# Optimization experiments

Hardware: AMD Instinct MI355X
Metric: run time of the kernel (lower is better)

## Reference

```python
import jax, jax.numpy as jnp
import numpy as np

STATE_MASS = 4.0
EPS = 1e-5
LOW_RANK_SCALE = 0.1  # _LOW_RANK_SCALE_INIT


def _ln(x, g, b):
    mu = jnp.mean(x, axis=-1, keepdims=True)
    var = jnp.var(x, axis=-1, keepdims=True)
    return (x - mu) * jax.lax.rsqrt(var + EPS) * g + b


def _signed_abs_softmax(s, axis=-1):
    s = jnp.nan_to_num(s)
    return jnp.sign(s) * jax.nn.softmax(jnp.abs(s), axis=axis)


def _signed_softmax_state(st):
    st = jnp.nan_to_num(st)
    return jnp.sign(st) * jax.nn.softmax(jnp.abs(st), axis=-1) * STATE_MASS


def _low_rank_scores(dst, src, Ut_w, Ut_b, Us_w, Us_b, w):
    # bilinear low-rank pairwise: score[b,i,j] = sum_r (dst_i Ut)_r * w_r * (src_j Us)_r
    pt = dst @ Ut_w + Ut_b                      # [B,Nd,R]
    ps = src @ Us_w + Us_b                      # [B,Ns,R]
    return jnp.einsum('bir,r,bjr->bij', pt, w * LOW_RANK_SCALE, ps)


def _gather_rows(x, idx):
    # x: [B,N,...], idx: [B,M,K] -> [B,M,K,...] (per-batch gather, no NxM broadcast)
    return jax.vmap(lambda xi, ii: xi[ii])(x, idx)


def setup_inputs() -> dict:
    key = jax.random.key(0)
    ks = jax.random.split(key, 8)
    B, S, D, M, R = 16, 2048, 512, 256, 64
    std = 0.02
    return {
        'token_val': jax.random.normal(ks[0], (B, S, D), jnp.float32),
        'token_state': jax.random.normal(ks[1], (B, S), jnp.float32),
        'init_state': jax.random.normal(ks[2], (M,), jnp.float32) * std,
        'init_val': jax.random.normal(ks[3], (M, D), jnp.float32) * std,
        'rUs_w': jax.random.normal(ks[4], (D, R), jnp.float32) * std,
        'rUs_b': jnp.zeros((R,), jnp.float32),
        'rUt_w': jax.random.normal(ks[5], (D, R), jnp.float32) * std,
        'rUt_b': jnp.zeros((R,), jnp.float32),
        'r_w': jnp.ones((R,), jnp.float32),
        'pUs_w': jax.random.normal(ks[6], (D, R), jnp.float32) * std,
        'pUs_b': jnp.zeros((R,), jnp.float32),
        'pUt_w': jax.random.normal(ks[7], (D, R), jnp.float32) * std,
        'pUt_b': jnp.zeros((R,), jnp.float32),
        'p_w': jnp.ones((R,), jnp.float32),
        'ln_g': jnp.ones((D,), jnp.float32),
        'ln_b': jnp.zeros((D,), jnp.float32),
        'topk': 16,
    }


def reference(token_val, token_state, init_state, init_val,
              rUs_w, rUs_b, rUt_w, rUt_b, r_w,
              pUs_w, pUs_b, pUt_w, pUt_b, p_w,
              ln_g, ln_b, topk):
    B = token_val.shape[0]
    M, D = init_val.shape

    # _MemoryLevel.initialize
    mem_state = _signed_softmax_state(jnp.broadcast_to(init_state, (B, M)))
    mem_val = _ln(jnp.broadcast_to(init_val, (B, M, D)), ln_g, ln_b)

    # ---- SparseTransition (write): route tokens -> slots, top-k sources/slot ----
    scores = _low_rank_scores(mem_val, token_val, rUt_w, rUt_b, rUs_w, rUs_b, r_w)  # [B,M,S]
    _, idx = jax.lax.top_k(jnp.abs(scores), topk)              # [B,M,K]
    sel = jnp.take_along_axis(scores, idx, axis=-1)            # [B,M,K]
    edges = _signed_abs_softmax(sel, axis=-1)                  # signed-abs-softmax over edges
    v_sel = _gather_rows(token_val, idx)                       # [B,M,K,D]
    s_sel = _gather_rows(token_state, idx)                     # [B,M,K]
    mem_val = mem_val + jnp.einsum('bmk,bmkd->bmd', edges, v_sel)   # merge_mode='add'
    mem_state = mem_state + jnp.einsum('bmk,bmk->bm', edges, s_sel)
    mem_state = _signed_softmax_state(mem_state)
    mem_val = _ln(mem_val, ln_g, ln_b)

    # ---- SparsePropagation within slots: state-weighted top-k edges, residual ----
    pscores = _low_rank_scores(mem_val, mem_val, pUt_w, pUt_b, pUs_w, pUs_b, p_w)   # [B,M,M]
    pscores = pscores * mem_state[:, None, :]                  # state_weight_edges
    _, pidx = jax.lax.top_k(jnp.abs(pscores), topk)            # [B,M,K]
    psel = jnp.take_along_axis(pscores, pidx, axis=-1)
    pe = _signed_abs_softmax(psel, axis=-1)
    pv = _gather_rows(mem_val, pidx)                           # [B,M,K,D]
    pst = _gather_rows(mem_state, pidx)                        # [B,M,K]
    mem_val = mem_val + jnp.einsum('bmk,bmkd->bmd', pe, pv)    # residual=True
    mem_state = mem_state + jnp.einsum('bmk,bmk->bm', pe, pst)
    mem_state = _signed_softmax_state(mem_state)
    mem_val = _ln(mem_val, ln_g, ln_b)
    return mem_val
```

## Files before the change

### kernel.cpp

```cpp
#include <hip/hip_runtime.h>
#include <hip/hip_bf16.h>
#include <math.h>

#define BB 16
#define SS 2048
#define DD 512
#define MM 256
#define RR 64
#define KK 16
#define GPAD 68

__device__ __forceinline__ float wave_sum(float v) {
#pragma unroll
  for (int off = 32; off > 0; off >>= 1) v += __shfl_xor(v, off);
  return v;
}

__device__ __forceinline__ float sgnf(float v) {
  return (v > 0.f) ? 1.f : ((v < 0.f) ? -1.f : 0.f);
}

__global__ __launch_bounds__(256) void k_init(
    const float* __restrict__ init_val, const float* __restrict__ ln_g,
    const float* __restrict__ ln_b, const float* __restrict__ rUt_w,
    const float* __restrict__ rUt_b, const float* __restrict__ r_w,
    float* __restrict__ mv0, float* __restrict__ pt0) {
  int m = blockIdx.x, t = threadIdx.x;
  __shared__ float row[DD];
  __shared__ float red[8];
  float x0 = init_val[m * DD + t];
  float x1 = init_val[m * DD + t + 256];
  float s = wave_sum(x0 + x1);
  float sq = wave_sum(x0 * x0 + x1 * x1);
  if ((t & 63) == 0) { red[t >> 6] = s; red[4 + (t >> 6)] = sq; }
  __syncthreads();
  float mean = (red[0] + red[1] + red[2] + red[3]) * (1.0f / DD);
  float var = (red[4] + red[5] + red[6] + red[7]) * (1.0f / DD) - mean * mean;
  float rs = rsqrtf(var + 1e-5f);
  float n0 = (x0 - mean) * rs * ln_g[t] + ln_b[t];
  float n1 = (x1 - mean) * rs * ln_g[t + 256] + ln_b[t + 256];
  mv0[m * DD + t] = n0;
  mv0[m * DD + t + 256] = n1;
  row[t] = n0;
  row[t + 256] = n1;
  __syncthreads();
  if (t < RR) {
    float acc = rUt_b[t];
    for (int d = 0; d < DD; ++d) acc += row[d] * rUt_w[d * RR + t];
    pt0[m * RR + t] = acc * r_w[t] * 0.1f;
  }
}

__global__ __launch_bounds__(256) void k_state_softmax(
    const float* __restrict__ in, float* __restrict__ out) {
  int b = blockIdx.x, t = threadIdx.x;
  __shared__ float red[4];
  float v = in[b * MM + t];
  float a = fabsf(v);
  float mx = a;
#pragma unroll
  for (int off = 32; off > 0; off >>= 1) mx = fmaxf(mx, __shfl_xor(mx, off));
  if ((t & 63) == 0) red[t >> 6] = mx;
  __syncthreads();
  mx = fmaxf(fmaxf(red[0], red[1]), fmaxf(red[2], red[3]));
  __syncthreads();
  float e = expf(a - mx);
  float ssum = wave_sum(e);
  if ((t & 63) == 0) red[t >> 6] = ssum;
  __syncthreads();
  ssum = red[0] + red[1] + red[2] + red[3];
  out[b * MM + t] = sgnf(v) * e / ssum * 4.0f;
}

__global__ __launch_bounds__(256) void k_ps(
    const float* __restrict__ A, const float* __restrict__ W,
    const float* __restrict__ bias, float* __restrict__ C0,
    float* __restrict__ C1) {
  __shared__ float Ast[32][256];
  __shared__ float Ws[32][RR];
  int t = threadIdx.x;
  int cg = t & 7;
  int rg = t >> 3;
  int half = blockIdx.x >> 7;
  int row0 = (blockIdx.x & 127) * 256;
  int k0 = half * 256;
  float* C = half ? C1 : C0;
  float4 ra[8];
  float4 rw[2];
#pragma unroll
  for (int i = 0; i < 8; ++i)
    ra[i] = *reinterpret_cast<const float4*>(
        &A[(size_t)(row0 + t) * DD + k0 + i * 4]);
#pragma unroll
  for (int i = 0; i < 2; ++i) {
    int slot = i * 256 + t;
    int k = slot >> 4, c4 = slot & 15;
    rw[i] = *reinterpret_cast<const float4*>(&W[(size_t)(k0 + k) * RR + c4 * 4]);
  }
  float acc[8][8] = {};
  for (int c = 0; c < 8; ++c) {
    __syncthreads();
#pragma unroll
    for (int i = 0; i < 8; ++i) {
      Ast[i * 4 + 0][t] = ra[i].x;
      Ast[i * 4 + 1][t] = ra[i].y;
      Ast[i * 4 + 2][t] = ra[i].z;
      Ast[i * 4 + 3][t] = ra[i].w;
    }
#pragma unroll
    for (int i = 0; i < 2; ++i) {
      int slot = i * 256 + t;
      int k = slot >> 4, c4 = slot & 15;
      *reinterpret_cast<float4*>(&Ws[k][c4 * 4]) = rw[i];
    }
    __syncthreads();
    if (c < 7) {
      int kc = k0 + (c + 1) * 32;
#pragma unroll
      for (int i = 0; i < 8; ++i)
        ra[i] = *reinterpret_cast<const float4*>(
            &A[(size_t)(row0 + t) * DD + kc + i * 4]);
#pragma unroll
      for (int i = 0; i < 2; ++i) {
        int slot = i * 256 + t;
        int k = slot >> 4, c4 = slot & 15;
        rw[i] = *reinterpret_cast<const float4*>(
            &W[(size_t)(kc + k) * RR + c4 * 4]);
      }
    }
#pragma unroll
    for (int k = 0; k < 32; ++k) {
      float4 a0 = *reinterpret_cast<const float4*>(&Ast[k][rg * 8]);
      float4 a1 = *reinterpret_cast<const float4*>(&Ast[k][rg * 8 + 4]);
      float4 w0 = *reinterpret_cast<const float4*>(&Ws[k][cg * 8]);
      float4 w1 = *reinterpret_cast<const float4*>(&Ws[k][cg * 8 + 4]);
      float av[8] = {a0.x, a0.y, a0.z, a0.w, a1.x, a1.y, a1.z, a1.w};
      float wv[8] = {w0.x, w0.y, w0.z, w0.w, w1.x, w1.y, w1.z, w1.w};
#pragma unroll
      for (int r = 0; r < 8; ++r)
#pragma unroll
        for (int cc = 0; cc < 8; ++cc) acc[r][cc] += av[r] * wv[cc];
    }
  }
  float bvx[8];
#pragma unroll
  for (int cc = 0; cc < 8; ++cc) bvx[cc] = (half == 0) ? bias[cg * 8 + cc] : 0.f;
#pragma unroll
  for (int r = 0; r < 8; ++r) {
    int rr = row0 + rg * 8 + r;
    float4 o0, o1;
    o0.x = acc[r][0] + bvx[0]; o0.y = acc[r][1] + bvx[1];
    o0.z = acc[r][2] + bvx[2]; o0.w = acc[r][3] + bvx[3];
    o1.x = acc[r][4] + bvx[4]; o1.y = acc[r][5] + bvx[5];
    o1.z = acc[r][6] + bvx[6]; o1.w = acc[r][7] + bvx[7];
    *reinterpret_cast<float4*>(&C[(size_t)rr * RR + cg * 8]) = o0;
    *reinterpret_cast<float4*>(&C[(size_t)rr * RR + cg * 8 + 4]) = o1;
  }
}

template <bool TRANS_OUT>
__device__ __forceinline__ void gemm_body(
    const float* __restrict__ A, const float* __restrict__ W,
    const float* __restrict__ bias, const float* __restrict__ colscale,
    float csmul, const float* __restrict__ rowscale, float* __restrict__ C,
    int row0, float (*Ast)[GPAD], float (*Ws)[GPAD]) {
  int tid = threadIdx.x;
  int ty = tid >> 4, tx = tid & 15;
  float acc[4][4] = {};
  for (int kc = 0; kc < DD; kc += 32) {
#pragma unroll
    for (int i = 0; i < 2; ++i) {
      int s4 = i * 256 + tid;
      int r = s4 >> 3;
      int k4 = s4 & 7;
      float4 v = *reinterpret_cast<const float4*>(
          &A[(size_t)(row0 + r) * DD + kc + k4 * 4]);
      Ast[k4 * 4 + 0][r] = v.x;
      Ast[k4 * 4 + 1][r] = v.y;
      Ast[k4 * 4 + 2][r] = v.z;
      Ast[k4 * 4 + 3][r] = v.w;
    }
#pragma unroll
    for (int i = 0; i < 2; ++i) {
      int s4 = i * 256 + tid;
      int r = s4 >> 4;
      int c4 = s4 & 15;
      float4 v = *reinterpret_cast<const float4*>(
          &W[(size_t)(kc + r) * RR + c4 * 4]);
      *reinterpret_cast<float4*>(&Ws[r][c4 * 4]) = v;
    }
    __syncthreads();
#pragma unroll
    for (int k = 0; k < 32; ++k) {
      float4 a4 = *reinterpret_cast<const float4*>(&Ast[k][ty * 4]);
      float4 w4 = *reinterpret_cast<const float4*>(&Ws[k][tx * 4]);
      acc[0][0] += a4.x * w4.x; acc[0][1] += a4.x * w4.y;
      acc[0][2] += a4.x * w4.z; acc[0][3] += a4.x * w4.w;
      acc[1][0] += a4.y * w4.x; acc[1][1] += a4.y * w4.y;
      acc[1][2] += a4.y * w4.z; acc[1][3] += a4.y * w4.w;
      acc[2][0] += a4.z * w4.x; acc[2][1] += a4.z * w4.y;
      acc[2][2] += a4.z * w4.z; acc[2][3] += a4.z * w4.w;
      acc[3][0] += a4.w * w4.x; acc[3][1] += a4.w * w4.y;
      acc[3][2] += a4.w * w4.z; acc[3][3] += a4.w * w4.w;
    }
    __syncthreads();
  }
#pragma unroll
  for (int i = 0; i < 4; ++i) {
    int rr = row0 + ty * 4 + i;
    float rsc = rowscale ? rowscale[rr] : 1.f;
#pragma unroll
    for (int j = 0; j < 4; ++j) {
      int cc = tx * 4 + j;
      float v = acc[i][j] + bias[cc];
      if (colscale) v *= colscale[cc] * csmul;
      v *= rsc;
      if (TRANS_OUT) {
        C[((size_t)(rr >> 8) * RR + cc) * MM + (rr & 255)] = v;
      } else {
        C[(size_t)rr * RR + cc] = v;
      }
    }
  }
}

__global__ __launch_bounds__(256) void k_gemm_pair(
    const float* __restrict__ mv1, const float* __restrict__ pUt_w,
    const float* __restrict__ pUt_b, const float* __restrict__ p_w,
    const float* __restrict__ pUs_w, const float* __restrict__ pUs_b,
    const float* __restrict__ ms1, float* __restrict__ pt1,
    float* __restrict__ ps1T) {
  __shared__ float Ast[32][GPAD];
  __shared__ float Ws[32][GPAD];
  if (blockIdx.x < 64) {
    gemm_body<false>(mv1, pUt_w, pUt_b, p_w, 0.1f, nullptr, pt1,
                     blockIdx.x * 64, Ast, Ws);
  } else {
    gemm_body<true>(mv1, pUs_w, pUs_b, nullptr, 1.f, ms1, ps1T,
                    (blockIdx.x - 64) * 64, Ast, Ws);
  }
}

#define PSW 144
__device__ __forceinline__ int psw(int j) { return j + ((j >> 5) << 2); }

__global__ __launch_bounds__(256) void k_scores(
    const float* __restrict__ pt0, const float* __restrict__ ps0,
    const float* __restrict__ ps1, float* __restrict__ scores) {
  __shared__ float PtT[RR][128];
  __shared__ float PsT[RR][PSW];
  int t = threadIdx.x;
  int b = blockIdx.z;
  int m0 = blockIdx.y * 128;
  int j0 = blockIdx.x * 128;
#pragma unroll
  for (int ii = 0; ii < 2; ++ii) {
    int slot = ii * 256 + t;
    int tm4 = slot >> 4, tk4 = slot & 15;
    const float* base = pt0 + (size_t)(m0 + tm4 * 4) * RR + tk4 * 4;
    float4 v0 = *reinterpret_cast<const float4*>(base);
    float4 v1 = *reinterpret_cast<const float4*>(base + RR);
    float4 v2 = *reinterpret_cast<const float4*>(base + 2 * RR);
    float4 v3 = *reinterpret_cast<const float4*>(base + 3 * RR);
    float4 w;
    w.x = v0.x; w.y = v1.x; w.z = v2.x; w.w = v3.x;
    *reinterpret_cast<float4*>(&PtT[tk4 * 4 + 0][tm4 * 4]) = w;
    w.x = v0.y; w.y = v1.y; w.z = v2.y; w.w = v3.y;
    *reinterpret_cast<float4*>(&PtT[tk4 * 4 + 1][tm4 * 4]) = w;
    w.x = v0.z; w.y = v1.z; w.z = v2.z; w.w = v3.z;
    *reinterpret_cast<float4*>(&PtT[tk4 * 4 + 2][tm4 * 4]) = w;
    w.x = v0.w; w.y = v1.w; w.z = v2.w; w.w = v3.w;
    *reinterpret_cast<float4*>(&PtT[tk4 * 4 + 3][tm4 * 4]) = w;
  }
#pragma unroll
  for (int ii = 0; ii < 2; ++ii) {
    int slot = ii * 256 + t;
    int jt = slot >> 4, kt = slot & 15;
    size_t off = ((size_t)b * SS + j0 + jt * 4) * RR + kt * 4;
    const float* base0 = ps0 + off;
    const float* base1 = ps1 + off;
    float4 v0 = *reinterpret_cast<const float4*>(base0);
    float4 v1 = *reinterpret_cast<const float4*>(base0 + RR);
    float4 v2 = *reinterpret_cast<const float4*>(base0 + 2 * RR);
    float4 v3 = *reinterpret_cast<const float4*>(base0 + 3 * RR);
    float4 u0 = *reinterpret_cast<const float4*>(base1);
    float4 u1 = *reinterpret_cast<const float4*>(base1 + RR);
    float4 u2 = *reinterpret_cast<const float4*>(base1 + 2 * RR);
    float4 u3 = *reinterpret_cast<const float4*>(base1 + 3 * RR);
    v0.x += u0.x; v0.y += u0.y; v0.z += u0.z; v0.w += u0.w;
    v1.x += u1.x; v1.y += u1.y; v1.z += u1.z; v1.w += u1.w;
    v2.x += u2.x; v2.y += u2.y; v2.z += u2.z; v2.w += u2.w;
    v3.x += u3.x; v3.y += u3.y; v3.z += u3.z; v3.w += u3.w;
    int jc = psw(jt * 4);
    float4 w;
    w.x = v0.x; w.y = v1.x; w.z = v2.x; w.w = v3.x;
    *reinterpret_cast<float4*>(&PsT[kt * 4 + 0][jc]) = w;
    w.x = v0.y; w.y = v1.y; w.z = v2.y; w.w = v3.y;
    *reinterpret_cast<float4*>(&PsT[kt * 4 + 1][jc]) = w;
    w.x = v0.z; w.y = v1.z; w.z = v2.z; w.w = v3.z;
    *reinterpret_cast<float4*>(&PsT[kt * 4 + 2][jc]) = w;
    w.x = v0.w; w.y = v1.w; w.z = v2.w; w.w = v3.w;
    *reinterpret_cast<float4*>(&PsT[kt * 4 + 3][jc]) = w;
  }
  __syncthreads();
  int jg = t & 15;
  int mg = t >> 4;
  int jlo = psw(jg * 8);
  float acc[8][8] = {};
#pragma unroll
  for (int k = 0; k < RR; ++k) {
    float4 a0 = *reinterpret_cast<const float4*>(&PtT[k][mg * 8]);
    float4 a1 = *reinterpret_cast<const float4*>(&PtT[k][mg * 8 + 4]);
    float4 w0 = *reinterpret_cast<const float4*>(&PsT[k][jlo]);
    float4 w1 = *reinterpret_cast<const float4*>(&PsT[k][jlo + 4]);
    float av[8] = {a0.x, a0.y, a0.z, a0.w, a1.x, a1.y, a1.z, a1.w};
    float wv[8] = {w0.x, w0.y, w0.z, w0.w, w1.x, w1.y, w1.z, w1.w};
#pragma unroll
    for (int r = 0; r < 8; ++r)
#pragma unroll
      for (int cc = 0; cc < 8; ++cc) acc[r][cc] += av[r] * wv[cc];
  }
  float* obase =
      scores + (size_t)b * MM * SS + (size_t)(m0 + mg * 8) * SS + j0 + jg * 8;
#pragma unroll
  for (int r = 0; r < 8; ++r) {
    float4 o0, o1;
    o0.x = acc[r][0]; o0.y = acc[r][1]; o0.z = acc[r][2]; o0.w = acc[r][3];
    o1.x = acc[r][4]; o1.y = acc[r][5]; o1.z = acc[r][6]; o1.w = acc[r][7];
    *reinterpret_cast<float4*>(obase + (size_t)r * SS) = o0;
    *reinterpret_cast<float4*>(obase + (size_t)r * SS + 4) = o1;
  }
}

__global__ __launch_bounds__(256) void k_write(
    const float* __restrict__ scores, const float* __restrict__ token_val,
    const float* __restrict__ token_state, const float* __restrict__ mv0,
    const float* __restrict__ ms0, const float* __restrict__ ln_g,
    const float* __restrict__ ln_b, float* __restrict__ mv1,
    float* __restrict__ ms_w) {
  int t = threadIdx.x;
  int wave = t >> 6, lane = t & 63;
  int i = blockIdx.x;
  int slot = i >> 3;
  int b = 2 * (i & 7) + (slot >> 6);
  int m = (slot & 63) * 4 + wave;
  int row = b * MM + m;
  __shared__ float srl[4][SS];
  __shared__ int selj_sh[4][KK];
  float4* srl4 = reinterpret_cast<float4*>(&srl[wave][0]);
  const float* srow = scores + (size_t)row * SS;
  unsigned au[32];
  unsigned maxa = 0u;
#pragma unroll
  for (int ch = 0; ch < 8; ++ch) {
    float4 q = *reinterpret_cast<const float4*>(srow + (ch * 64 + lane) * 4);
    srl4[ch * 64 + lane] = q;
    au[ch * 4 + 0] = __float_as_uint(q.x) & 0x7fffffffu;
    au[ch * 4 + 1] = __float_as_uint(q.y) & 0x7fffffffu;
    au[ch * 4 + 2] = __float_as_uint(q.z) & 0x7fffffffu;
    au[ch * 4 + 3] = __float_as_uint(q.w) & 0x7fffffffu;
    maxa = max(maxa, max(max(au[ch * 4], au[ch * 4 + 1]),
                         max(au[ch * 4 + 2], au[ch * 4 + 3])));
  }
#pragma unroll
  for (int off = 32; off > 0; off >>= 1)
    maxa = max(maxa, (unsigned)__shfl_xor((int)maxa, off));
  unsigned lo = 0u, hi = maxa, thr = 0u;
  bool early = false;
  while (lo < hi) {
    unsigned mid = lo + ((hi - lo + 1u) >> 1);
    int cnt = 0;
#pragma unroll
    for (int c = 0; c < 32; ++c) cnt += __popcll(__ballot(au[c] >= mid));
    if (cnt == KK) { thr = mid; early = true; break; }
    if (cnt > KK) lo = mid; else hi = mid - 1u;
  }
  if (!early) thr = lo;
  unsigned long long ltmask = (1ull << lane) - 1ull;
  int s = 0;
  unsigned tiemask = 0u;
#pragma unroll
  for (int c = 0; c < 32; ++c) {
    bool sg = early ? (au[c] >= thr) : (au[c] > thr);
    unsigned long long mk = __ballot(sg);
    if (sg)
      selj_sh[wave][s + __popcll(mk & ltmask)] =
          (c >> 2) * 256 + lane * 4 + (c & 3);
    s += __popcll(mk);
    if (!early && au[c] == thr) tiemask |= 1u << c;
  }
  int taken = s;
  while (taken < KK) {
    int myj = 0x7fffffff;
#pragma unroll
    for (int c = 0; c < 32; ++c)
      if ((tiemask >> c) & 1u) {
        int j = (c >> 2) * 256 + lane * 4 + (c & 3);
        myj = min(myj, j);
      }
    int wj = myj;
#pragma unroll
    for (int off = 32; off > 0; off >>= 1) wj = min(wj, __shfl_xor(wj, off));
    if (wj == 0x7fffffff) break;
    if (((wj >> 2) & 63) == lane) tiemask &= ~(1u << (((wj >> 8) << 2) | (wj & 3)));
    if (lane == 0) selj_sh[wave][taken] = wj;
    ++taken;
  }
  int js[KK];
  float es[KK];
#pragma unroll
  for (int k = 0; k < KK; ++k) {
    js[k] = selj_sh[wave][k];
    es[k] = srl[wave][js[k]];
  }
  float mx = 0.f;
#pragma unroll
  for (int k = 0; k < KK; ++k) mx = fmaxf(mx, fabsf(es[k]));
  float ssum = 0.f;
#pragma unroll
  for (int k = 0; k < KK; ++k) {
    float ex = expf(fabsf(es[k]) - mx);
    ssum += ex;
    es[k] = sgnf(es[k]) * ex;
  }
  float inv = 1.f / ssum;
  int dbase = lane * 8;
  const float* m0row = mv0 + m * DD + dbase;
  float4 a0 = *reinterpret_cast<const float4*>(m0row);
  float4 a1 = *reinterpret_cast<const float4*>(m0row + 4);
  float acc[8] = {a0.x, a0.y, a0.z, a0.w, a1.x, a1.y, a1.z, a1.w};
  float stacc = 0.f;
#pragma unroll
  for (int k = 0; k < KK; ++k) {
    float e = es[k] * inv;
    const float* tv = token_val + ((size_t)b * SS + js[k]) * DD + dbase;
    float4 u0 = *reinterpret_cast<const float4*>(tv);
    float4 u1 = *reinterpret_cast<const float4*>(tv + 4);
    acc[0] += e * u0.x; acc[1] += e * u0.y; acc[2] += e * u0.z; acc[3] += e * u0.w;
    acc[4] += e * u1.x; acc[5] += e * u1.y; acc[6] += e * u1.z; acc[7] += e * u1.w;
    stacc += e * token_state[(size_t)b * SS + js[k]];
  }
  if (lane == 0) ms_w[row] = ms0[m] + stacc;
  float s1 = 0.f, s2 = 0.f;
#pragma unroll
  for (int c = 0; c < 8; ++c) { s1 += acc[c]; s2 += acc[c] * acc[c]; }
  s1 = wave_sum(s1);
  s2 = wave_sum(s2);
  float mean = s1 * (1.0f / DD);
  float var = s2 * (1.0f / DD) - mean * mean;
  float rs = rsqrtf(var + 1e-5f);
  float4 g0 = *reinterpret_cast<const float4*>(ln_g + dbase);
  float4 g1 = *reinterpret_cast<const float4*>(ln_g + dbase + 4);
  float4 b0v = *reinterpret_cast<const float4*>(ln_b + dbase);
  float4 b1v = *reinterpret_cast<const float4*>(ln_b + dbase + 4);
  float4 o0, o1;
  o0.x = (acc[0] - mean) * rs * g0.x + b0v.x;
  o0.y = (acc[1] - mean) * rs * g0.y + b0v.y;
  o0.z = (acc[2] - mean) * rs * g0.z + b0v.z;
  o0.w = (acc[3] - mean) * rs * g0.w + b0v.w;
  o1.x = (acc[4] - mean) * rs * g1.x + b1v.x;
  o1.y = (acc[5] - mean) * rs * g1.y + b1v.y;
  o1.z = (acc[6] - mean) * rs * g1.z + b1v.z;
  o1.w = (acc[7] - mean) * rs * g1.w + b1v.w;
  float* orow = mv1 + (size_t)row * DD + dbase;
  *reinterpret_cast<float4*>(orow) = o0;
  *reinterpret_cast<float4*>(orow + 4) = o1;
}

__global__ __launch_bounds__(256, 4) void k_prop(
    const float* __restrict__ pt1, const float* __restrict__ ps1T,
    const float* __restrict__ mv1, const float* __restrict__ ln_g,
    const float* __restrict__ ln_b, float* __restrict__ out) {
  int t = threadIdx.x;
  int wave = t >> 6, lane = t & 63;
  int row = blockIdx.x * 4 + wave;
  int b = row >> 8, m = row & 255;
  __shared__ int selj_sh[4][KK];
  __shared__ float selv_sh[4][KK];
  float ptval = pt1[(size_t)row * RR + lane];
  const float* pB = ps1T + (size_t)b * RR * MM + lane * 4;
  float sc[4] = {0.f, 0.f, 0.f, 0.f};
#pragma unroll 8
  for (int r = 0; r < RR; ++r) {
    float w = __shfl(ptval, r);
    float4 pv = *reinterpret_cast<const float4*>(pB + r * MM);
    sc[0] += w * pv.x; sc[1] += w * pv.y; sc[2] += w * pv.z; sc[3] += w * pv.w;
  }
  int jbase = lane * 4;
  unsigned au[4];
#pragma unroll
  for (int c = 0; c < 4; ++c) au[c] = __float_as_uint(sc[c]) & 0x7fffffffu;
  unsigned lo = 0u, hi = 0x7f800000u, thr = 0u;
  bool early = false;
  while (lo < hi) {
    unsigned mid = lo + ((hi - lo + 1u) >> 1);
    int cnt = 0;
#pragma unroll
    for (int c = 0; c < 4; ++c) cnt += __popcll(__ballot(au[c] >= mid));
    if (cnt == KK) { thr = mid; early = true; break; }
    if (cnt > KK) lo = mid; else hi = mid - 1u;
  }
  if (!early) thr = lo;
  unsigned long long ltmask = (1ull << lane) - 1ull;
  int s = 0;
  unsigned tiemask = 0u;
#pragma unroll
  for (int c = 0; c < 4; ++c) {
    bool sg = early ? (au[c] >= thr) : (au[c] > thr);
    unsigned long long mk = __ballot(sg);
    if (sg) {
      int slot = s + __popcll(mk & ltmask);
      selj_sh[wave][slot] = jbase + c;
      selv_sh[wave][slot] = sc[c];
    }
    s += __popcll(mk);
    if (!early && au[c] == thr) tiemask |= 1u << c;
  }
  int taken = s;
  while (taken < KK) {
    int myj = 0x7fffffff;
#pragma unroll
    for (int c = 0; c < 4; ++c)
      if ((tiemask >> c) & 1u) myj = min(myj, jbase + c);
    int wj = myj;
#pragma unroll
    for (int off = 32; off > 0; off >>= 1) wj = min(wj, __shfl_xor(wj, off));
    if (wj == 0x7fffffff) break;
    if (wj >= jbase && wj < jbase + 4) {
      tiemask &= ~(1u << (wj - jbase));
      selv_sh[wave][taken] = sc[wj - jbase];
      if (lane == (wj >> 2)) selj_sh[wave][taken] = wj;
    }
    ++taken;
  }
  int js[KK];
  float es[KK];
#pragma unroll
  for (int k = 0; k < KK; ++k) { js[k] = selj_sh[wave][k]; es[k] = selv_sh[wave][k]; }
  float mx = 0.f;
#pragma unroll
  for (int k = 0; k < KK; ++k) mx = fmaxf(mx, fabsf(es[k]));
  float ssum = 0.f;
#pragma unroll
  for (int k = 0; k < KK; ++k) {
    float ex = expf(fabsf(es[k]) - mx);
    ssum += ex;
    es[k] = sgnf(es[k]) * ex;
  }
  float inv = 1.f / ssum;
  int dbase = lane * 8;
  const float* mrow = mv1 + (size_t)row * DD + dbase;
  float4 a0 = *reinterpret_cast<const float4*>(mrow);
  float4 a1 = *reinterpret_cast<const float4*>(mrow + 4);
  float acc[8] = {a0.x, a0.y, a0.z, a0.w, a1.x, a1.y, a1.z, a1.w};
#pragma unroll
  for (int k = 0; k < KK; ++k) {
    float e = es[k] * inv;
    const float* pv = mv1 + ((size_t)b * MM + js[k]) * DD + dbase;
    float4 u0 = *reinterpret_cast<const float4*>(pv);
    float4 u1 = *reinterpret_cast<const float4*>(pv + 4);
    acc[0] += e * u0.x; acc[1] += e * u0.y; acc[2] += e * u0.z; acc[3] += e * u0.w;
    acc[4] += e * u1.x; acc[5] += e * u1.y; acc[6] += e * u1.z; acc[7] += e * u1.w;
  }
  float s1 = 0.f, s2 = 0.f;
#pragma unroll
  for (int c = 0; c < 8; ++c) { s1 += acc[c]; s2 += acc[c] * acc[c]; }
  s1 = wave_sum(s1);
  s2 = wave_sum(s2);
  float mean = s1 * (1.0f / DD);
  float var = s2 * (1.0f / DD) - mean * mean;
  float rs = rsqrtf(var + 1e-5f);
  float4 g0 = *reinterpret_cast<const float4*>(ln_g + dbase);
  float4 g1 = *reinterpret_cast<const float4*>(ln_g + dbase + 4);
  float4 b0v = *reinterpret_cast<const float4*>(ln_b + dbase);
  float4 b1v = *reinterpret_cast<const float4*>(ln_b + dbase + 4);
  float4 o0, o1;
  o0.x = (acc[0] - mean) * rs * g0.x + b0v.x;
  o0.y = (acc[1] - mean) * rs * g0.y + b0v.y;
  o0.z = (acc[2] - mean) * rs * g0.z + b0v.z;
  o0.w = (acc[3] - mean) * rs * g0.w + b0v.w;
  o1.x = (acc[4] - mean) * rs * g1.x + b1v.x;
  o1.y = (acc[5] - mean) * rs * g1.y + b1v.y;
  o1.z = (acc[6] - mean) * rs * g1.z + b1v.z;
  o1.w = (acc[7] - mean) * rs * g1.w + b1v.w;
  float* orow = out + (size_t)row * DD + dbase;
  *reinterpret_cast<float4*>(orow) = o0;
  *reinterpret_cast<float4*>(orow + 4) = o1;
}

extern "C" void kernel_launch(void* const* d_in, const int* in_sizes, int n_in,
                              void* d_out, int out_size, void* d_ws,
                              size_t ws_size, hipStream_t stream) {
  const float* token_val = (const float*)d_in[0];
  const float* token_state = (const float*)d_in[1];
  const float* init_state = (const float*)d_in[2];
  const float* init_val = (const float*)d_in[3];
  const float* rUs_w = (const float*)d_in[4];
  const float* rUs_b = (const float*)d_in[5];
  const float* rUt_w = (const float*)d_in[6];
  const float* rUt_b = (const float*)d_in[7];
  const float* r_w = (const float*)d_in[8];
  const float* pUs_w = (const float*)d_in[9];
  const float* pUs_b = (const float*)d_in[10];
  const float* pUt_w = (const float*)d_in[11];
  const float* pUt_b = (const float*)d_in[12];
  const float* p_w = (const float*)d_in[13];
  const float* ln_g = (const float*)d_in[14];
  const float* ln_b = (const float*)d_in[15];
  float* out = (float*)d_out;

  float* ws = (float*)d_ws;
  float* mv0 = ws;    ws += MM * DD;
  float* pt0 = ws;    ws += MM * RR;
  float* ms0 = ws;    ws += MM;
  float* ps = ws;     ws += (size_t)BB * SS * RR;
  float* scores = ws; ws += (size_t)BB * MM * SS;
  float* mv1 = ws;    ws += (size_t)BB * MM * DD;
  float* ms_w = ws;   ws += BB * MM;
  float* ms1 = ws;    ws += BB * MM;
  float* pt1 = ws;    ws += (size_t)BB * MM * RR;
  float* ps1T = ws;   ws += (size_t)BB * RR * MM;
  float* psB = mv1;

  k_init<<<MM, 256, 0, stream>>>(init_val, ln_g, ln_b, rUt_w, rUt_b, r_w, mv0, pt0);
  k_state_softmax<<<1, 256, 0, stream>>>(init_state, ms0);
  k_ps<<<256, 256, 0, stream>>>(token_val, rUs_w, rUs_b, ps, psB);
  dim3 gs(SS / 128, MM / 128, BB);
  k_scores<<<gs, 256, 0, stream>>>(pt0, ps, psB, scores);
  k_write<<<(BB * MM) / 4, 256, 0, stream>>>(scores, token_val, token_state,
                                             mv0, ms0, ln_g, ln_b, mv1, ms_w);
  k_state_softmax<<<BB, 256, 0, stream>>>(ms_w, ms1);
  k_gemm_pair<<<128, 256, 0, stream>>>(mv1, pUt_w, pUt_b, p_w, pUs_w, pUs_b,
                                       ms1, pt1, ps1T);
  k_prop<<<(BB * MM) / 4, 256, 0, stream>>>(pt1, ps1T, mv1, ln_g, ln_b, out);
}
```

Before: 172.9 us.

## Stream k_ps tiles directly into LDS with double buffering and swizzled layout

Rewrites the token projection GEMM (k_ps) to use 128-thread blocks over 128-row tiles. The A and W tiles are now fetched with global_load_lds straight into a double-buffered LDS stage, instead of through registers followed by transposed LDS stores. Loads are arranged so eight consecutive lanes cover one row's 32-float chunk, which improves coalescing over the old one-row-per-thread stride. A XOR swizzle on the A tile avoids LDS bank conflicts when each thread reads its 8 rows. The design relies on the barrier also waiting for the asynchronous LDS DMA to finish. It also doubles the grid size and halves the threads per block.

```diff
diff --git a/kernel.cpp b/kernel.cpp
--- a/kernel.cpp
+++ b/kernel.cpp
@@ -72,87 +72,95 @@
   out[b * MM + t] = sgnf(v) * e / ssum * 4.0f;
 }
 
-__global__ __launch_bounds__(256) void k_ps(
+__global__ __launch_bounds__(128) void k_ps(
     const float* __restrict__ A, const float* __restrict__ W,
     const float* __restrict__ bias, float* __restrict__ C0,
     float* __restrict__ C1) {
-  __shared__ float Ast[32][256];
-  __shared__ float Ws[32][RR];
+  __shared__ float Abuf[2][128 * 32];
+  __shared__ float Wbuf[2][32 * RR];
   int t = threadIdx.x;
-  int cg = t & 7;
-  int rg = t >> 3;
-  int half = blockIdx.x >> 7;
-  int row0 = (blockIdx.x & 127) * 256;
+  int half = blockIdx.x >> 8;
+  int row0 = (blockIdx.x & 255) * 128;
   int k0 = half * 256;
   float* C = half ? C1 : C0;
-  float4 ra[8];
-  float4 rw[2];
-#pragma unroll
-  for (int i = 0; i < 8; ++i)
-    ra[i] = *reinterpret_cast<const float4*>(
-        &A[(size_t)(row0 + t) * DD + k0 + i * 4]);
-#pragma unroll
-  for (int i = 0; i < 2; ++i) {
-    int slot = i * 256 + t;
-    int k = slot >> 4, c4 = slot & 15;
-    rw[i] = *reinterpret_cast<const float4*>(&W[(size_t)(k0 + k) * RR + c4 * 4]);
-  }
+  int rg = t >> 3;
+  int cg = t & 7;
+  int sw = rg & 7;
+
+  auto stage = [&](int buf, int c) {
+    int kc = k0 + c * 32;
+#pragma unroll
+    for (int i = 0; i < 8; ++i) {
+      int d = i * 128 + t;
+      int row = d >> 3, cl = d & 7;
+      int cgs = cl ^ ((row >> 3) & 7);
+      const float* src = A + (size_t)(row0 + row) * DD + kc + cgs * 4;
+      __builtin_amdgcn_global_load_lds(
+          (const __attribute__((address_space(1))) void*)src,
+          (__attribute__((address_space(3))) void*)(&Abuf[buf][d * 4]),
+          16, 0, 0);
+    }
+#pragma unroll
+    for (int i = 0; i < 4; ++i) {
+      int d = i * 128 + t;
+      const float* src = W + (size_t)kc * RR + d * 4;
+      __builtin_amdgcn_global_load_lds(
+          (const __attribute__((address_space(1))) void*)src,
+          (__attribute__((address_space(3))) void*)(&Wbuf[buf][d * 4]),
+          16, 0, 0);
+    }
+  };
+
   float acc[8][8] = {};
+  stage(0, 0);
   for (int c = 0; c < 8; ++c) {
     __syncthreads();
-#pragma unroll
-    for (int i = 0; i < 8; ++i) {
-      Ast[i * 4 + 0][t] = ra[i].x;
-      Ast[i * 4 + 1][t] = ra[i].y;
-      Ast[i * 4 + 2][t] = ra[i].z;
-      Ast[i * 4 + 3][t] = ra[i].w;
-    }
-#pragma unroll
-    for (int i = 0; i < 2; ++i) {
-      int slot = i * 256 + t;
-      int k = slot >> 4, c4 = slot & 15;
-      *reinterpret_cast<float4*>(&Ws[k][c4 * 4]) = rw[i];
-    }
-    __syncthreads();
-    if (c < 7) {
-      int kc = k0 + (c + 1) * 32;
-#pragma unroll
-      for (int i = 0; i < 8; ++i)
-        ra[i] = *reinterpret_cast<const float4*>(
-            &A[(size_t)(row0 + t) * DD + kc + i * 4]);
-#pragma unroll
-      for (int i = 0; i < 2; ++i) {
-        int slot = i * 256 + t;
-        int k = slot >> 4, c4 = slot & 15;
-        rw[i] = *reinterpret_cast<const float4*>(
-            &W[(size_t)(kc + k) * RR + c4 * 4]);
+    if (c < 7) stage((c + 1) & 1, c + 1);
+    const float* Ab = &Abuf[c & 1][0];
+    const float* Wb = &Wbuf[c & 1][0];
+#pragma unroll
+    for (int kq = 0; kq < 8; ++kq) {
+      float4 a4[8];
+#pragma unroll
+      for (int i = 0; i < 8; ++i) {
+        int row = rg * 8 + i;
+        a4[i] = *reinterpret_cast<const float4*>(
+            Ab + row * 32 + ((kq ^ sw) * 4));
       }
-    }
-#pragma unroll
-    for (int k = 0; k < 32; ++k) {
-      float4 a0 = *reinterpret_cast<const float4*>(&Ast[k][rg * 8]);
-      float4 a1 = *reinterpret_cast<const float4*>(&Ast[k][rg * 8 + 4]);
-      float4 w0 = *reinterpret_cast<const float4*>(&Ws[k][cg * 8]);
-      float4 w1 = *reinterpret_cast<const float4*>(&Ws[k][cg * 8 + 4]);
-      float av[8] = {a0.x, a0.y, a0.z, a0.w, a1.x, a1.y, a1.z, a1.w};
-      float wv[8] = {w0.x, w0.y, w0.z, w0.w, w1.x, w1.y, w1.z, w1.w};
-#pragma unroll
-      for (int r = 0; r < 8; ++r)
-#pragma unroll
-        for (int cc = 0; cc < 8; ++cc) acc[r][cc] += av[r] * wv[cc];
+      float4 wlo[4], whi[4];
+#pragma unroll
+      for (int k2 = 0; k2 < 4; ++k2) {
+        wlo[k2] = *reinterpret_cast<const float4*>(
+            Wb + (kq * 4 + k2) * RR + cg * 8);
+        whi[k2] = *reinterpret_cast<const float4*>(
+            Wb + (kq * 4 + k2) * RR + cg * 8 + 4);
+      }
+#pragma unroll
+      for (int k2 = 0; k2 < 4; ++k2) {
+        float wv[8] = {wlo[k2].x, wlo[k2].y, wlo[k2].z, wlo[k2].w,
+                       whi[k2].x, whi[k2].y, whi[k2].z, whi[k2].w};
+#pragma unroll
+        for (int i = 0; i < 8; ++i) {
+          float av = (k2 == 0) ? a4[i].x
+                   : (k2 == 1) ? a4[i].y
+                   : (k2 == 2) ? a4[i].z : a4[i].w;
+#pragma unroll
+          for (int j = 0; j < 8; ++j) acc[i][j] += av * wv[j];
+        }
+      }
     }
   }
   float bvx[8];
 #pragma unroll
-  for (int cc = 0; cc < 8; ++cc) bvx[cc] = (half == 0) ? bias[cg * 8 + cc] : 0.f;
-#pragma unroll
-  for (int r = 0; r < 8; ++r) {
-    int rr = row0 + rg * 8 + r;
+  for (int j = 0; j < 8; ++j) bvx[j] = (half == 0) ? bias[cg * 8 + j] : 0.f;
+#pragma unroll
+  for (int i = 0; i < 8; ++i) {
+    int rr = row0 + rg * 8 + i;
     float4 o0, o1;
-    o0.x = acc[r][0] + bvx[0]; o0.y = acc[r][1] + bvx[1];
-    o0.z = acc[r][2] + bvx[2]; o0.w = acc[r][3] + bvx[3];
-    o1.x = acc[r][4] + bvx[4]; o1.y = acc[r][5] + bvx[5];
-    o1.z = acc[r][6] + bvx[6]; o1.w = acc[r][7] + bvx[7];
+    o0.x = acc[i][0] + bvx[0]; o0.y = acc[i][1] + bvx[1];
+    o0.z = acc[i][2] + bvx[2]; o0.w = acc[i][3] + bvx[3];
+    o1.x = acc[i][4] + bvx[4]; o1.y = acc[i][5] + bvx[5];
+    o1.z = acc[i][6] + bvx[6]; o1.w = acc[i][7] + bvx[7];
     *reinterpret_cast<float4*>(&C[(size_t)rr * RR + cg * 8]) = o0;
     *reinterpret_cast<float4*>(&C[(size_t)rr * RR + cg * 8 + 4]) = o1;
   }
@@ -624,7 +632,7 @@
 
   k_init<<<MM, 256, 0, stream>>>(init_val, ln_g, ln_b, rUt_w, rUt_b, r_w, mv0, pt0);
   k_state_softmax<<<1, 256, 0, stream>>>(init_state, ms0);
-  k_ps<<<256, 256, 0, stream>>>(token_val, rUs_w, rUs_b, ps, psB);
+  k_ps<<<512, 128, 0, stream>>>(token_val, rUs_w, rUs_b, ps, psB);
   dim3 gs(SS / 128, MM / 128, BB);
   k_scores<<<gs, 256, 0, stream>>>(pt0, ps, psB, scores);
   k_write<<<(BB * MM) / 4, 256, 0, stream>>>(scores, token_val, token_state,
```

Measured after the change: 169.2 us. 1.02x faster.
